# Performance work log

Measured on AMD Instinct MI355X. Metric: run time of the kernel, lower is better.

The kernel has to match this reference:

```python
import jax, jax.numpy as jnp
import numpy as np

N = 50000          # num_nodes
F_IN = 128         # node_features
H = 256            # hidden_dim
H_OUT = H // 2     # 128
E = 800000         # num_edges (avg degree 16)
LN_EPS = 1e-5


def _glorot(key, fan_in, fan_out):
    lim = np.sqrt(6.0 / (fan_in + fan_out))
    return jax.random.uniform(key, (fan_in, fan_out), jnp.float32, -lim, lim)


def setup_inputs() -> dict:
    key = jax.random.key(0)
    ks = jax.random.split(key, 8)
    node_ids = jnp.arange(N, dtype=jnp.int64 if jax.config.jax_enable_x64 else jnp.int32)
    edge_index = jax.random.randint(ks[0], (2, E), 0, N, dtype=jnp.int32)
    emb = jax.random.normal(ks[1], (N, F_IN), jnp.float32)
    W1 = _glorot(ks[2], F_IN, H)
    b1 = jnp.zeros((H,), jnp.float32)
    W2 = _glorot(ks[3], H, H)
    b2 = jnp.zeros((H,), jnp.float32)
    W3 = _glorot(ks[4], H, H_OUT)
    b3 = jnp.zeros((H_OUT,), jnp.float32)
    gamma = jnp.ones((H_OUT,), jnp.float32)
    beta = jnp.zeros((H_OUT,), jnp.float32)
    return {"node_ids": node_ids, "edge_index": edge_index, "emb": emb,
            "W1": W1, "b1": b1, "W2": W2, "b2": b2, "W3": W3, "b3": b3,
            "gamma": gamma, "beta": beta}


def _gcn_norm(edge_index):
    # PyG GCNConv default: add self-loops, symmetric normalization D^-1/2 A D^-1/2
    loop = jnp.arange(N, dtype=edge_index.dtype)
    src = jnp.concatenate([edge_index[0], loop])  # [E + N]
    dst = jnp.concatenate([edge_index[1], loop])
    deg = jax.ops.segment_sum(jnp.ones_like(dst, jnp.float32), dst, num_segments=N)
    dinv = jnp.where(deg > 0, jax.lax.rsqrt(deg), 0.0)
    norm = dinv[src] * dinv[dst]  # [E + N]
    return src, dst, norm


def _gcn_conv(x, src, dst, norm, W, b):
    h = x @ W                               # [N, d_out] transform first (PyG order)
    msg = h[src] * norm[:, None]            # gather + scale  [E+N, d_out]
    out = jax.ops.segment_sum(msg, dst, num_segments=N)  # scatter-add
    return out + b


def _layer_norm(x, gamma, beta):
    mu = jnp.mean(x, axis=-1, keepdims=True)
    var = jnp.mean(jnp.square(x - mu), axis=-1, keepdims=True)
    return (x - mu) * jax.lax.rsqrt(var + LN_EPS) * gamma + beta


def reference(node_ids, edge_index, emb, W1, b1, W2, b2, W3, b3, gamma, beta):
    src, dst, norm = _gcn_norm(edge_index)
    x = emb[node_ids]                       # embedding lookup [N, F_IN]
    x = jax.nn.relu(_gcn_conv(x, src, dst, norm, W1, b1))
    # dropout is identity in eval mode
    x = jax.nn.relu(_gcn_conv(x, src, dst, norm, W2, b2))
    x = _gcn_conv(x, src, dst, norm, W3, b3)
    return _layer_norm(x, gamma, beta)
```

## Files before the change

kernel.cpp:

```cpp
#include <hip/hip_runtime.h>
#include <hip/hip_bf16.h>


#define BLK 256

typedef __attribute__((ext_vector_type(8))) short bf16x8;
typedef __attribute__((ext_vector_type(4))) float f32x4;
typedef unsigned short u16;
typedef unsigned int u32;

__device__ inline u16 f2b_rne(float v) {
    u32 x = __float_as_uint(v);
    u32 r = (x + 0x7FFFu + ((x >> 16) & 1u)) >> 16;
    return (u16)r;
}
__device__ inline void split_bf(float v, u16& h, u16& l) {
    h = f2b_rne(v);
    float fh = __uint_as_float((u32)h << 16);
    l = f2b_rne(v - fh);
}

__global__ void k_indeg(const int* __restrict__ dst, int* __restrict__ indeg, int E) {
    int e = blockIdx.x * blockDim.x + threadIdx.x;
    if (e < E) atomicAdd(&indeg[dst[e]], 1);
}

#define SCAN_T 1024
__global__ void k_scan(const int* __restrict__ indeg, int* __restrict__ rowptr, int n) {
    __shared__ int s_wsum[16];
    __shared__ int s_wpre[16];
    __shared__ int s_carry;
    int tid = threadIdx.x, lane = tid & 63, wid = tid >> 6;
    if (tid == 0) s_carry = 0;
    __syncthreads();
    const int CHUNK = SCAN_T * 8;
    for (int base = 0; base < n; base += CHUNK) {
        int idx0 = base + tid * 8;
        int loc[8]; int lsum = 0;
#pragma unroll
        for (int j = 0; j < 8; ++j) {
            int idx = idx0 + j;
            loc[j] = (idx < n) ? indeg[idx] : 0;
            lsum += loc[j];
        }
        int sc = lsum;
#pragma unroll
        for (int off = 1; off < 64; off <<= 1) {
            int t = __shfl_up(sc, off, 64);
            if (lane >= off) sc += t;
        }
        if (lane == 63) s_wsum[wid] = sc;
        __syncthreads();
        if (tid < 16) {
            int w = s_wsum[tid];
#pragma unroll
            for (int off = 1; off < 16; off <<= 1) {
                int t = __shfl_up(w, off, 64);
                if (tid >= off) w += t;
            }
            s_wpre[tid] = w;
        }
        __syncthreads();
        int excl = s_carry + (wid ? s_wpre[wid - 1] : 0) + sc - lsum;
#pragma unroll
        for (int j = 0; j < 8; ++j) {
            int idx = idx0 + j;
            if (idx < n) rowptr[idx] = excl;
            excl += loc[j];
        }
        __syncthreads();
        if (tid == 0) s_carry += s_wpre[15];
    }
    if (tid == 0) rowptr[n] = s_carry;
}

__global__ void k_fill(const int* __restrict__ src, const int* __restrict__ dst,
                       const int* __restrict__ rowptr, int* __restrict__ cursor,
                       int* __restrict__ col, int E) {
    int e = blockIdx.x * blockDim.x + threadIdx.x;
    if (e < E) {
        int d = dst[e];
        int pos = rowptr[d] + atomicAdd(&cursor[d], 1);
        col[pos] = src[e];
    }
}

__global__ void k_dinv(const int* __restrict__ indeg, float* __restrict__ dinv, int n) {
    int i = blockIdx.x * blockDim.x + threadIdx.x;
    if (i < n) dinv[i] = rsqrtf((float)indeg[i] + 1.0f);
}

__global__ void k_wprep(const float* __restrict__ W, u16* __restrict__ Whi,
                        u16* __restrict__ Wlo, int K, int N) {
    int idx = blockIdx.x * blockDim.x + threadIdx.x;
    if (idx >= K * N) return;
    int nn = idx / K, kk = idx - nn * K;
    float v = W[(size_t)kk * N + nn];
    u16 h, l; split_bf(v, h, l);
    Whi[idx] = h; Wlo[idx] = l;
}

__global__ void k_prescale(const float* __restrict__ emb, const int* __restrict__ ids,
                           const float* __restrict__ dinv, float* __restrict__ xs, int n) {
    int t = blockIdx.x * blockDim.x + threadIdx.x;
    if (t >= n * 32) return;
    int node = t >> 5, lane = t & 31;
    int s = ids[node];
    float4 v = ((const float4*)emb)[(size_t)s * 32 + lane];
    float di = dinv[node];
    ((float4*)xs)[(size_t)node * 32 + lane] = make_float4(v.x*di, v.y*di, v.z*di, v.w*di);
}

template<int D, int EPI, int OUT>
__global__ __launch_bounds__(BLK) void k_agg(const float* __restrict__ H,
        const int* __restrict__ rowptr, const int* __restrict__ col,
        const float* __restrict__ dinv, const float* __restrict__ bias,
        float* __restrict__ outf, u16* __restrict__ outh, u16* __restrict__ outl, int n) {
    constexpr int LPN = D / 4;
    int t = blockIdx.x * blockDim.x + threadIdx.x;
    int node = t / LPN;
    int lane = t % LPN;
    if (node >= n) return;
    const float4* Hv = (const float4*)H;
    float4 acc = Hv[(size_t)node * LPN + lane];
    int e = rowptr[node], end = rowptr[node + 1];
    for (; e + 4 <= end; e += 4) {
        int s0 = col[e], s1 = col[e+1], s2 = col[e+2], s3 = col[e+3];
        float4 v0 = Hv[(size_t)s0 * LPN + lane];
        float4 v1 = Hv[(size_t)s1 * LPN + lane];
        float4 v2 = Hv[(size_t)s2 * LPN + lane];
        float4 v3 = Hv[(size_t)s3 * LPN + lane];
        acc.x += (v0.x + v1.x) + (v2.x + v3.x);
        acc.y += (v0.y + v1.y) + (v2.y + v3.y);
        acc.z += (v0.z + v1.z) + (v2.z + v3.z);
        acc.w += (v0.w + v1.w) + (v2.w + v3.w);
    }
    for (; e < end; ++e) {
        int s = col[e];
        float4 v = Hv[(size_t)s * LPN + lane];
        acc.x += v.x; acc.y += v.y; acc.z += v.z; acc.w += v.w;
    }
    float di = dinv[node];
    float4 r;
    if constexpr (EPI == 0) {
        r = make_float4(acc.x*di, acc.y*di, acc.z*di, acc.w*di);
    } else {
        float4 b = ((const float4*)bias)[lane];
        r.x = fmaxf(fmaf(acc.x, di, b.x), 0.f);
        r.y = fmaxf(fmaf(acc.y, di, b.y), 0.f);
        r.z = fmaxf(fmaf(acc.z, di, b.z), 0.f);
        r.w = fmaxf(fmaf(acc.w, di, b.w), 0.f);
    }
    if constexpr (OUT == 0) {
        ((float4*)outf)[(size_t)node * LPN + lane] = r;
    } else {
        ushort4 h4, l4;
        split_bf(r.x, h4.x, l4.x);
        split_bf(r.y, h4.y, l4.y);
        split_bf(r.z, h4.z, l4.z);
        split_bf(r.w, h4.w, l4.w);
        ((ushort4*)outh)[(size_t)node * LPN + lane] = h4;
        ((ushort4*)outl)[(size_t)node * LPN + lane] = l4;
    }
}

__global__ __launch_bounds__(BLK) void k_agg_ln(const float* __restrict__ H,
        const int* __restrict__ rowptr, const int* __restrict__ col,
        const float* __restrict__ dinv, const float* __restrict__ b3,
        const float* __restrict__ gamma, const float* __restrict__ beta,
        float* __restrict__ out, int n) {
    int gt = blockIdx.x * blockDim.x + threadIdx.x;
    int node = gt >> 6;
    int lane = gt & 63;
    if (node >= n) return;
    const float2* Hv = (const float2*)H;
    float2 acc = Hv[(size_t)node * 64 + lane];
    int e = rowptr[node], end = rowptr[node + 1];
    for (; e + 4 <= end; e += 4) {
        int s0 = col[e], s1 = col[e+1], s2 = col[e+2], s3 = col[e+3];
        float2 v0 = Hv[(size_t)s0 * 64 + lane];
        float2 v1 = Hv[(size_t)s1 * 64 + lane];
        float2 v2 = Hv[(size_t)s2 * 64 + lane];
        float2 v3 = Hv[(size_t)s3 * 64 + lane];
        acc.x += (v0.x + v1.x) + (v2.x + v3.x);
        acc.y += (v0.y + v1.y) + (v2.y + v3.y);
    }
    for (; e < end; ++e) {
        int s = col[e];
        float2 v = Hv[(size_t)s * 64 + lane];
        acc.x += v.x; acc.y += v.y;
    }
    float di = dinv[node];
    int f0 = lane * 2;
    float t0 = fmaf(acc.x, di, b3[f0]);
    float t1 = fmaf(acc.y, di, b3[f0 + 1]);
    float s = t0 + t1, sq = t0*t0 + t1*t1;
#pragma unroll
    for (int off = 32; off >= 1; off >>= 1) {
        s  += __shfl_xor(s, off, 64);
        sq += __shfl_xor(sq, off, 64);
    }
    float mu  = s * (1.0f / 128.0f);
    float var = sq * (1.0f / 128.0f) - mu * mu;
    float inv = rsqrtf(var + 1e-5f);
    float2 o;
    o.x = fmaf((t0 - mu) * inv, gamma[f0],     beta[f0]);
    o.y = fmaf((t1 - mu) * inv, gamma[f0 + 1], beta[f0 + 1]);
    ((float2*)out)[(size_t)node * 64 + lane] = o;
}

template<int EPI>
__global__ __launch_bounds__(256) void k_gemm_bf3(
        const u16* __restrict__ Ahi, const u16* __restrict__ Alo,
        const u16* __restrict__ Bhi, const u16* __restrict__ Blo,
        const float* __restrict__ bias, const float* __restrict__ dinv,
        float* __restrict__ Cf, u16* __restrict__ Chi, u16* __restrict__ Clo,
        int M, int N, int K) {
    __shared__ u16 sA[2][128 * 64];
    __shared__ u16 sB[2][128 * 64];
    int m0 = blockIdx.x * 128;
    int n0 = blockIdx.y * 128;
    int tid = threadIdx.x;
    int lane = tid & 63, wid = tid >> 6;
    int wm = wid >> 1, wn = wid & 1;
    int r16 = lane & 15, kg = lane >> 4;
    f32x4 acc[4][4] = {};
    for (int k0 = 0; k0 < K; k0 += 64) {
        for (int c = tid; c < 1024; c += 256) {
            int row = c >> 3, slot = c & 7;
            int sl = slot ^ (row & 7);
            int gm = m0 + row;
            uint4 vh = make_uint4(0u,0u,0u,0u), vl = vh;
            if (gm < M) {
                size_t g = (size_t)gm * K + k0 + slot * 8;
                vh = *(const uint4*)(Ahi + g);
                vl = *(const uint4*)(Alo + g);
            }
            *(uint4*)&sA[0][row * 64 + sl * 8] = vh;
            *(uint4*)&sA[1][row * 64 + sl * 8] = vl;
            size_t gb = (size_t)(n0 + row) * K + k0 + slot * 8;
            *(uint4*)&sB[0][row * 64 + sl * 8] = *(const uint4*)(Bhi + gb);
            *(uint4*)&sB[1][row * 64 + sl * 8] = *(const uint4*)(Blo + gb);
        }
        __syncthreads();
#pragma unroll
        for (int kk = 0; kk < 2; ++kk) {
            bf16x8 ah[4], al[4], bh[4], bl[4];
#pragma unroll
            for (int f = 0; f < 4; ++f) {
                int ar = wm * 64 + f * 16 + r16;
                int asl = (kk * 4 + kg) ^ (ar & 7);
                ah[f] = *(const bf16x8*)&sA[0][ar * 64 + asl * 8];
                al[f] = *(const bf16x8*)&sA[1][ar * 64 + asl * 8];
                int br = wn * 64 + f * 16 + r16;
                int bsl = (kk * 4 + kg) ^ (br & 7);
                bh[f] = *(const bf16x8*)&sB[0][br * 64 + bsl * 8];
                bl[f] = *(const bf16x8*)&sB[1][br * 64 + bsl * 8];
            }
#pragma unroll
            for (int i = 0; i < 4; ++i)
#pragma unroll
            for (int j = 0; j < 4; ++j) {
                acc[i][j] = __builtin_amdgcn_mfma_f32_16x16x32_bf16(ah[i], bh[j], acc[i][j], 0, 0, 0);
                acc[i][j] = __builtin_amdgcn_mfma_f32_16x16x32_bf16(ah[i], bl[j], acc[i][j], 0, 0, 0);
                acc[i][j] = __builtin_amdgcn_mfma_f32_16x16x32_bf16(al[i], bh[j], acc[i][j], 0, 0, 0);
            }
        }
        __syncthreads();
    }
#pragma unroll
    for (int i = 0; i < 4; ++i) {
#pragma unroll
        for (int j = 0; j < 4; ++j) {
            int nn = n0 + wn * 64 + j * 16 + r16;
            float bv = 0.f;
            if constexpr (EPI == 0) bv = bias[nn];
#pragma unroll
            for (int r = 0; r < 4; ++r) {
                int mm = m0 + wm * 64 + i * 16 + kg * 4 + r;
                if (mm >= M) continue;
                float x = acc[i][j][r];
                if constexpr (EPI == 0) {
                    x = fmaxf(x + bv, 0.f);
                    u16 h, l; split_bf(x, h, l);
                    size_t o = (size_t)mm * N + nn;
                    Chi[o] = h; Clo[o] = l;
                } else {
                    x *= dinv[mm];
                    Cf[(size_t)mm * N + nn] = x;
                }
            }
        }
    }
}

static inline size_t align256(size_t x) { return (x + 255) & ~(size_t)255; }

extern "C" void kernel_launch(void* const* d_in, const int* in_sizes, int n_in,
                              void* d_out, int out_size, void* d_ws, size_t ws_size,
                              hipStream_t stream) {
    const int*   node_ids = (const int*)  d_in[0];
    const int*   ei       = (const int*)  d_in[1];
    const float* emb      = (const float*)d_in[2];
    const float* W1       = (const float*)d_in[3];
    const float* b1       = (const float*)d_in[4];
    const float* W2       = (const float*)d_in[5];
    const float* b2       = (const float*)d_in[6];
    const float* W3       = (const float*)d_in[7];
    const float* b3       = (const float*)d_in[8];
    const float* gamma    = (const float*)d_in[9];
    const float* beta     = (const float*)d_in[10];
    float* out = (float*)d_out;

    const int N = in_sizes[0];
    const int E = in_sizes[1] / 2;
    const int* esrc = ei;
    const int* edst = ei + E;

    char* p = (char*)d_ws;
    size_t off = 0;
    int*   indeg  = (int*)(p + off);   off = align256(off + (size_t)N * 4);
    int*   rowptr = (int*)(p + off);   off = align256(off + (size_t)(N + 1) * 4);
    int*   cursor = (int*)(p + off);   off = align256(off + (size_t)N * 4);
    float* dinv   = (float*)(p + off); off = align256(off + (size_t)N * 4);
    int*   col    = (int*)(p + off);   off = align256(off + (size_t)E * 4);
    u16* W1thi = (u16*)(p + off); off = align256(off + 256 * 128 * 2);
    u16* W1tlo = (u16*)(p + off); off = align256(off + 256 * 128 * 2);
    u16* W2thi = (u16*)(p + off); off = align256(off + 256 * 256 * 2);
    u16* W2tlo = (u16*)(p + off); off = align256(off + 256 * 256 * 2);
    u16* W3thi = (u16*)(p + off); off = align256(off + 128 * 256 * 2);
    u16* W3tlo = (u16*)(p + off); off = align256(off + 128 * 256 * 2);
    char* S1 = p + off; off = align256(off + (size_t)N * 256 * 4);
    char* S2 = p + off; off = align256(off + (size_t)N * 256 * 4);

    float* X    = (float*)S1;
    u16*   H1hi = (u16*)S1;
    u16*   H1lo = (u16*)(S1 + (size_t)N * 256 * 2);
    u16*   X2hi = H1hi;
    u16*   X2lo = H1lo;
    u16*   A1hi = (u16*)S2;
    u16*   A1lo = (u16*)(S2 + (size_t)N * 128 * 2);
    float* G2   = (float*)S2;
    float* G3   = (float*)S2;

    hipMemsetAsync(indeg, 0, (size_t)N * 4, stream);
    hipMemsetAsync(cursor, 0, (size_t)N * 4, stream);

    int eb = (E + BLK - 1) / BLK;
    k_indeg<<<eb, BLK, 0, stream>>>(edst, indeg, E);
    k_scan<<<1, SCAN_T, 0, stream>>>(indeg, rowptr, N);
    k_fill<<<eb, BLK, 0, stream>>>(esrc, edst, rowptr, cursor, col, E);
    k_dinv<<<(N + BLK - 1) / BLK, BLK, 0, stream>>>(indeg, dinv, N);

    k_wprep<<<(128 * 256 + 255) / 256, 256, 0, stream>>>(W1, W1thi, W1tlo, 128, 256);
    k_wprep<<<(256 * 256 + 255) / 256, 256, 0, stream>>>(W2, W2thi, W2tlo, 256, 256);
    k_wprep<<<(256 * 128 + 255) / 256, 256, 0, stream>>>(W3, W3thi, W3tlo, 256, 128);

    int mg = (N + 127) / 128;

    k_prescale<<<(N * 32 + BLK - 1) / BLK, BLK, 0, stream>>>(emb, node_ids, dinv, X, N);
    k_agg<128, 0, 1><<<(N * 32 + BLK - 1) / BLK, BLK, 0, stream>>>(
        X, rowptr, col, dinv, nullptr, nullptr, A1hi, A1lo, N);
    k_gemm_bf3<0><<<dim3(mg, 2), 256, 0, stream>>>(
        A1hi, A1lo, W1thi, W1tlo, b1, nullptr, nullptr, H1hi, H1lo, N, 256, 128);
    k_gemm_bf3<1><<<dim3(mg, 2), 256, 0, stream>>>(
        H1hi, H1lo, W2thi, W2tlo, nullptr, dinv, G2, nullptr, nullptr, N, 256, 256);
    k_agg<256, 1, 1><<<(N * 64 + BLK - 1) / BLK, BLK, 0, stream>>>(
        G2, rowptr, col, dinv, b2, nullptr, X2hi, X2lo, N);
    k_gemm_bf3<1><<<dim3(mg, 1), 256, 0, stream>>>(
        X2hi, X2lo, W3thi, W3tlo, nullptr, dinv, G3, nullptr, nullptr, N, 128, 256);
    k_agg_ln<<<(N * 64 + BLK - 1) / BLK, BLK, 0, stream>>>(
        G3, rowptr, col, dinv, b3, gamma, beta, out, N);
}
```

Before: 586.2 us.

## Store aggregation inputs in 16-feature panels for cache-local gathers

```diff
diff --git a/kernel.cpp b/kernel.cpp
--- a/kernel.cpp
+++ b/kernel.cpp
@@ -104,97 +104,70 @@
                            const float* __restrict__ dinv, float* __restrict__ xs, int n) {
     int t = blockIdx.x * blockDim.x + threadIdx.x;
     if (t >= n * 32) return;
-    int node = t >> 5, lane = t & 31;
+    int node = t >> 5, fq = t & 31;
     int s = ids[node];
-    float4 v = ((const float4*)emb)[(size_t)s * 32 + lane];
+    float4 v = ((const float4*)emb)[(size_t)s * 32 + fq];
     float di = dinv[node];
-    ((float4*)xs)[(size_t)node * 32 + lane] = make_float4(v.x*di, v.y*di, v.z*di, v.w*di);
-}
-
-template<int D, int EPI, int OUT>
-__global__ __launch_bounds__(BLK) void k_agg(const float* __restrict__ H,
-        const int* __restrict__ rowptr, const int* __restrict__ col,
-        const float* __restrict__ dinv, const float* __restrict__ bias,
-        float* __restrict__ outf, u16* __restrict__ outh, u16* __restrict__ outl, int n) {
-    constexpr int LPN = D / 4;
-    int t = blockIdx.x * blockDim.x + threadIdx.x;
-    int node = t / LPN;
-    int lane = t % LPN;
-    if (node >= n) return;
-    const float4* Hv = (const float4*)H;
-    float4 acc = Hv[(size_t)node * LPN + lane];
-    int e = rowptr[node], end = rowptr[node + 1];
-    for (; e + 4 <= end; e += 4) {
-        int s0 = col[e], s1 = col[e+1], s2 = col[e+2], s3 = col[e+3];
-        float4 v0 = Hv[(size_t)s0 * LPN + lane];
-        float4 v1 = Hv[(size_t)s1 * LPN + lane];
-        float4 v2 = Hv[(size_t)s2 * LPN + lane];
-        float4 v3 = Hv[(size_t)s3 * LPN + lane];
-        acc.x += (v0.x + v1.x) + (v2.x + v3.x);
-        acc.y += (v0.y + v1.y) + (v2.y + v3.y);
-        acc.z += (v0.z + v1.z) + (v2.z + v3.z);
-        acc.w += (v0.w + v1.w) + (v2.w + v3.w);
-    }
-    for (; e < end; ++e) {
-        int s = col[e];
-        float4 v = Hv[(size_t)s * LPN + lane];
-        acc.x += v.x; acc.y += v.y; acc.z += v.z; acc.w += v.w;
-    }
-    float di = dinv[node];
-    float4 r;
-    if constexpr (EPI == 0) {
-        r = make_float4(acc.x*di, acc.y*di, acc.z*di, acc.w*di);
-    } else {
-        float4 b = ((const float4*)bias)[lane];
-        r.x = fmaxf(fmaf(acc.x, di, b.x), 0.f);
-        r.y = fmaxf(fmaf(acc.y, di, b.y), 0.f);
-        r.z = fmaxf(fmaf(acc.z, di, b.z), 0.f);
-        r.w = fmaxf(fmaf(acc.w, di, b.w), 0.f);
-    }
-    if constexpr (OUT == 0) {
-        ((float4*)outf)[(size_t)node * LPN + lane] = r;
-    } else {
-        ushort4 h4, l4;
-        split_bf(r.x, h4.x, l4.x);
-        split_bf(r.y, h4.y, l4.y);
-        split_bf(r.z, h4.z, l4.z);
-        split_bf(r.w, h4.w, l4.w);
-        ((ushort4*)outh)[(size_t)node * LPN + lane] = h4;
-        ((ushort4*)outl)[(size_t)node * LPN + lane] = l4;
-    }
-}
-
-__global__ __launch_bounds__(BLK) void k_agg_ln(const float* __restrict__ H,
-        const int* __restrict__ rowptr, const int* __restrict__ col,
-        const float* __restrict__ dinv, const float* __restrict__ b3,
+    int panel = fq >> 2, q = fq & 3;
+    ((float4*)xs)[((size_t)panel * n + node) * 4 + q] =
+        make_float4(v.x*di, v.y*di, v.z*di, v.w*di);
+}
+
+template<int NP, int EPI, int OUT>
+__global__ __launch_bounds__(256) void k_agg_p(
+        const float* __restrict__ Hs, const int* __restrict__ rowptr,
+        const int* __restrict__ col, const float* __restrict__ dinv,
+        const float* __restrict__ bias, float* __restrict__ outf,
+        u16* __restrict__ outh, u16* __restrict__ outl, int n) {
+    constexpr int NPW = 4;
+    int panel = blockIdx.y;
+    int lane = threadIdx.x & 63;
+    int wid  = blockIdx.x * (blockDim.x >> 6) + (threadIdx.x >> 6);
+    int esub = lane >> 4, fl = lane & 15;
+    const float* Hp = Hs + (size_t)panel * n * 16;
+    int node0 = wid * NPW;
+    for (int ni = 0; ni < NPW; ++ni) {
+        int node = node0 + ni;
+        if (node >= n) break;
+        int beg = rowptr[node], end = rowptr[node + 1];
+        float selfv = Hp[(size_t)node * 16 + fl];
+        float acc = 0.f;
+#pragma unroll 2
+        for (int e = beg; e < end; e += 4) {
+            int ee = e + esub;
+            int idx = col[min(ee, end - 1)];
+            float v = Hp[(size_t)idx * 16 + fl];
+            acc += (ee < end) ? v : 0.f;
+        }
+        acc += __shfl_xor(acc, 16, 64);
+        acc += __shfl_xor(acc, 32, 64);
+        acc += selfv;
+        float di = dinv[node];
+        int feat = panel * 16 + fl;
+        float r;
+        if constexpr (EPI == 0)      r = acc * di;
+        else if constexpr (EPI == 1) r = fmaxf(fmaf(acc, di, bias[feat]), 0.f);
+        else                         r = fmaf(acc, di, bias[feat]);
+        if (esub == 0) {
+            if constexpr (OUT == 0) {
+                outf[(size_t)node * (NP * 16) + feat] = r;
+            } else {
+                u16 h, l; split_bf(r, h, l);
+                outh[(size_t)node * (NP * 16) + feat] = h;
+                outl[(size_t)node * (NP * 16) + feat] = l;
+            }
+        }
+    }
+}
+
+__global__ __launch_bounds__(BLK) void k_ln(const float* __restrict__ T,
         const float* __restrict__ gamma, const float* __restrict__ beta,
         float* __restrict__ out, int n) {
     int gt = blockIdx.x * blockDim.x + threadIdx.x;
-    int node = gt >> 6;
-    int lane = gt & 63;
+    int node = gt >> 6, lane = gt & 63;
     if (node >= n) return;
-    const float2* Hv = (const float2*)H;
-    float2 acc = Hv[(size_t)node * 64 + lane];
-    int e = rowptr[node], end = rowptr[node + 1];
-    for (; e + 4 <= end; e += 4) {
-        int s0 = col[e], s1 = col[e+1], s2 = col[e+2], s3 = col[e+3];
-        float2 v0 = Hv[(size_t)s0 * 64 + lane];
-        float2 v1 = Hv[(size_t)s1 * 64 + lane];
-        float2 v2 = Hv[(size_t)s2 * 64 + lane];
-        float2 v3 = Hv[(size_t)s3 * 64 + lane];
-        acc.x += (v0.x + v1.x) + (v2.x + v3.x);
-        acc.y += (v0.y + v1.y) + (v2.y + v3.y);
-    }
-    for (; e < end; ++e) {
-        int s = col[e];
-        float2 v = Hv[(size_t)s * 64 + lane];
-        acc.x += v.x; acc.y += v.y;
-    }
-    float di = dinv[node];
-    int f0 = lane * 2;
-    float t0 = fmaf(acc.x, di, b3[f0]);
-    float t1 = fmaf(acc.y, di, b3[f0 + 1]);
-    float s = t0 + t1, sq = t0*t0 + t1*t1;
+    float2 t = ((const float2*)T)[(size_t)node * 64 + lane];
+    float s = t.x + t.y, sq = t.x*t.x + t.y*t.y;
 #pragma unroll
     for (int off = 32; off >= 1; off >>= 1) {
         s  += __shfl_xor(s, off, 64);
@@ -203,9 +176,10 @@
     float mu  = s * (1.0f / 128.0f);
     float var = sq * (1.0f / 128.0f) - mu * mu;
     float inv = rsqrtf(var + 1e-5f);
+    int f0 = lane * 2;
     float2 o;
-    o.x = fmaf((t0 - mu) * inv, gamma[f0],     beta[f0]);
-    o.y = fmaf((t1 - mu) * inv, gamma[f0 + 1], beta[f0 + 1]);
+    o.x = fmaf((t.x - mu) * inv, gamma[f0],     beta[f0]);
+    o.y = fmaf((t.y - mu) * inv, gamma[f0 + 1], beta[f0 + 1]);
     ((float2*)out)[(size_t)node * 64 + lane] = o;
 }
 
@@ -287,7 +261,7 @@
                     Chi[o] = h; Clo[o] = l;
                 } else {
                     x *= dinv[mm];
-                    Cf[(size_t)mm * N + nn] = x;
+                    Cf[((size_t)(nn >> 4) * M + mm) * 16 + (nn & 15)] = x;
                 }
             }
         }
@@ -330,18 +304,19 @@
     u16* W2tlo = (u16*)(p + off); off = align256(off + 256 * 256 * 2);
     u16* W3thi = (u16*)(p + off); off = align256(off + 128 * 256 * 2);
     u16* W3tlo = (u16*)(p + off); off = align256(off + 128 * 256 * 2);
-    char* S1 = p + off; off = align256(off + (size_t)N * 256 * 4);
-    char* S2 = p + off; off = align256(off + (size_t)N * 256 * 4);
-
-    float* X    = (float*)S1;
-    u16*   H1hi = (u16*)S1;
-    u16*   H1lo = (u16*)(S1 + (size_t)N * 256 * 2);
-    u16*   X2hi = H1hi;
-    u16*   X2lo = H1lo;
-    u16*   A1hi = (u16*)S2;
-    u16*   A1lo = (u16*)(S2 + (size_t)N * 128 * 2);
-    float* G2   = (float*)S2;
-    float* G3   = (float*)S2;
+    char* P1 = p + off; off = align256(off + (size_t)N * 256 * 4);
+    char* P2 = p + off; off = align256(off + (size_t)N * 256 * 4);
+
+    float* Xslab = (float*)P1;
+    u16*   H1hi  = (u16*)P1;
+    u16*   H1lo  = (u16*)(P1 + (size_t)N * 256 * 2);
+    u16*   X2hi  = H1hi;
+    u16*   X2lo  = H1lo;
+    float* T3    = (float*)P1;
+    u16*   A1hi  = (u16*)P2;
+    u16*   A1lo  = (u16*)(P2 + (size_t)N * 128 * 2);
+    float* G2s   = (float*)P2;
+    float* G3s   = (float*)P2;
 
     hipMemsetAsync(indeg, 0, (size_t)N * 4, stream);
     hipMemsetAsync(cursor, 0, (size_t)N * 4, stream);
@@ -357,18 +332,20 @@
     k_wprep<<<(256 * 128 + 255) / 256, 256, 0, stream>>>(W3, W3thi, W3tlo, 256, 128);
 
     int mg = (N + 127) / 128;
-
-    k_prescale<<<(N * 32 + BLK - 1) / BLK, BLK, 0, stream>>>(emb, node_ids, dinv, X, N);
-    k_agg<128, 0, 1><<<(N * 32 + BLK - 1) / BLK, BLK, 0, stream>>>(
-        X, rowptr, col, dinv, nullptr, nullptr, A1hi, A1lo, N);
+    int ab = (N + 15) / 16;
+
+    k_prescale<<<(N * 32 + BLK - 1) / BLK, BLK, 0, stream>>>(emb, node_ids, dinv, Xslab, N);
+    k_agg_p<8, 0, 1><<<dim3(ab, 8), BLK, 0, stream>>>(
+        Xslab, rowptr, col, dinv, nullptr, nullptr, A1hi, A1lo, N);
     k_gemm_bf3<0><<<dim3(mg, 2), 256, 0, stream>>>(
         A1hi, A1lo, W1thi, W1tlo, b1, nullptr, nullptr, H1hi, H1lo, N, 256, 128);
     k_gemm_bf3<1><<<dim3(mg, 2), 256, 0, stream>>>(
-        H1hi, H1lo, W2thi, W2tlo, nullptr, dinv, G2, nullptr, nullptr, N, 256, 256);
-    k_agg<256, 1, 1><<<(N * 64 + BLK - 1) / BLK, BLK, 0, stream>>>(
-        G2, rowptr, col, dinv, b2, nullptr, X2hi, X2lo, N);
+        H1hi, H1lo, W2thi, W2tlo, nullptr, dinv, G2s, nullptr, nullptr, N, 256, 256);
+    k_agg_p<16, 1, 1><<<dim3(ab, 16), BLK, 0, stream>>>(
+        G2s, rowptr, col, dinv, b2, nullptr, X2hi, X2lo, N);
     k_gemm_bf3<1><<<dim3(mg, 1), 256, 0, stream>>>(
-        X2hi, X2lo, W3thi, W3tlo, nullptr, dinv, G3, nullptr, nullptr, N, 128, 256);
-    k_agg_ln<<<(N * 64 + BLK - 1) / BLK, BLK, 0, stream>>>(
-        G3, rowptr, col, dinv, b3, gamma, beta, out, N);
-}
+        X2hi, X2lo, W3thi, W3tlo, nullptr, dinv, G3s, nullptr, nullptr, N, 128, 256);
+    k_agg_p<8, 2, 0><<<dim3(ab, 8), BLK, 0, stream>>>(
+        G3s, rowptr, col, dinv, b3, T3, nullptr, nullptr, N);
+    k_ln<<<(N * 64 + BLK - 1) / BLK, BLK, 0, stream>>>(T3, gamma, beta, out, N);
+}
```

Measured after the change: 865.7 us. 1.48x slower.
